# Performance work log

Measured on AMD Instinct MI355X. Metric: run time of the kernel, lower is better.

## Reference

```python
import jax, jax.numpy as jnp
import numpy as np

NEG = -1e30  # finite stand-in for -inf so softmax grads stay clean


def setup_inputs() -> dict:
    key = jax.random.key(0)
    k1, k2 = jax.random.split(key)
    C, D = 8192, 512
    gt_class_embeddings = jax.random.normal(k1, (C, D), dtype=jnp.float32)
    w = jax.random.normal(k2, (C, D), dtype=jnp.float32)
    return {"gt_class_embeddings": gt_class_embeddings, "w": w}


def reference(gt_class_embeddings, w):
    # L2-normalize class embeddings, cosine-similarity matrix S (diag == 1)
    G = gt_class_embeddings / jnp.linalg.norm(gt_class_embeddings, axis=-1, keepdims=True)
    S = G @ G.T  # [C, C]
    C = S.shape[0]
    off_diag = ~jnp.eye(C, dtype=bool)

    # seSoftmax: per-row softmax over entries != 1 (off-diagonal); diagonal stays 1
    P = jax.nn.softmax(jnp.where(off_diag, S, NEG), axis=-1)
    S2 = jnp.where(off_diag, P, 1.0)

    # argsort(-S2)[1] == most similar (diag value 1 always ranks first),
    # argsort(-S2)[-1] == least similar == row min (softmax values < 1)
    ms = jnp.argmax(jnp.where(off_diag, S2, NEG), axis=-1)  # [C]
    ls = jnp.argmin(jnp.where(off_diag, S2, -NEG), axis=-1)  # [C]

    rows = jnp.arange(C)
    margin = S2[rows, ms] - S2[rows, ls]  # [C]

    d_ms = jnp.sqrt(jnp.sum((w - w[ms]) ** 2, axis=-1))  # [C]
    d_ls = jnp.sqrt(jnp.sum((w - w[ls]) ** 2, axis=-1))  # [C]

    loss = jnp.mean(jnp.maximum(0.0, d_ms - d_ls + margin))
    return loss
```

## Files before the change

kernel.cpp:

```cpp
#include <hip/hip_runtime.h>
#include <math.h>

#define CDIM 8192
#define DDIM 512
#define NEGF -3.0e38f
#define POSF  3.0e38f

#define BM 128
#define NSLOT (CDIM / BM)

typedef __attribute__((ext_vector_type(8))) short bf16x8;
typedef __attribute__((ext_vector_type(4))) float f32x4;

__device__ __forceinline__ unsigned short f2bf(float x) {
    unsigned int u = __float_as_uint(x);
    u += 0x7fffu + ((u >> 16) & 1u);
    return (unsigned short)(u >> 16);
}
__device__ __forceinline__ float bf2f(unsigned short h) {
    return __uint_as_float(((unsigned int)h) << 16);
}
__device__ __forceinline__ void gld16(const void* g, void* l) {
    __builtin_amdgcn_global_load_lds(
        (__attribute__((address_space(1))) void*)(void*)g,
        (__attribute__((address_space(3))) void*)l, 16, 0, 0);
}

__global__ __launch_bounds__(256) void k_prep(const float* __restrict__ g,
                                              unsigned short* __restrict__ hi,
                                              unsigned short* __restrict__ lo) {
    const int wave = threadIdx.x >> 6;
    const int lane = threadIdx.x & 63;
    const int row = blockIdx.x * 4 + wave;
    const float4* src = (const float4*)(g + (size_t)row * DDIM);
    const float4 a = src[lane * 2];
    const float4 b = src[lane * 2 + 1];
    float s = a.x * a.x + a.y * a.y + a.z * a.z + a.w * a.w +
              b.x * b.x + b.y * b.y + b.z * b.z + b.w * b.w;
#pragma unroll
    for (int m = 1; m < 64; m <<= 1) s += __shfl_xor(s, m, 64);
    const float rn = rsqrtf(s);
    const float y[8] = {a.x * rn, a.y * rn, a.z * rn, a.w * rn,
                        b.x * rn, b.y * rn, b.z * rn, b.w * rn};
    unsigned int hv[4], lv[4];
#pragma unroll
    for (int i = 0; i < 4; ++i) {
        const unsigned short h0 = f2bf(y[2 * i]);
        const unsigned short h1 = f2bf(y[2 * i + 1]);
        const unsigned short l0 = f2bf(y[2 * i] - bf2f(h0));
        const unsigned short l1 = f2bf(y[2 * i + 1] - bf2f(h1));
        hv[i] = (unsigned int)h0 | ((unsigned int)h1 << 16);
        lv[i] = (unsigned int)l0 | ((unsigned int)l1 << 16);
    }
    uint4* dh = (uint4*)(hi + (size_t)row * DDIM + lane * 8);
    uint4* dl = (uint4*)(lo + (size_t)row * DDIM + lane * 8);
    *dh = make_uint4(hv[0], hv[1], hv[2], hv[3]);
    *dl = make_uint4(lv[0], lv[1], lv[2], lv[3]);
}

__global__ __launch_bounds__(256, 3) void k_simstats(
    const unsigned short* __restrict__ ghi, const unsigned short* __restrict__ glo,
    float* __restrict__ pmax, float* __restrict__ pmin, float* __restrict__ pZ,
    int* __restrict__ pamax, int* __restrict__ pamin) {
    __shared__ unsigned short SH[4 * BM * 32];
    unsigned short* Ahi = SH;
    unsigned short* Alo = SH + 4096;
    unsigned short* Bhi = SH + 8192;
    unsigned short* Blo = SH + 12288;
    const int t = threadIdx.x;
    const int wave = t >> 6;
    const int lane = t & 63;
    const int lanelo = lane & 15;
    const int quad = lane >> 4;
    const int wr = wave & 1;
    const int wc = wave >> 1;

    const int bid = blockIdx.x;
    const int xcd = bid & 7;
    const int off = bid >> 3;
    int I, J, ntiles;
    if (off < 4) {
        const int d = xcd * 4 + off;
        I = 2 * d; J = I; ntiles = 2;
    } else {
        const int e = xcd * 252 + (off - 4);
        int Jf = (int)((1.0f + sqrtf(1.0f + 8.0f * (float)e)) * 0.5f);
        while ((Jf * (Jf - 1)) / 2 > e) --Jf;
        while (((Jf + 1) * Jf) / 2 <= e) ++Jf;
        J = Jf; I = e - (Jf * (Jf - 1)) / 2;
        ntiles = 1;
    }

    const int srow = t >> 2;
    const int scolb = ((t & 3) ^ ((t >> 3) & 3)) << 4;
    char* lAh = (char*)Ahi + t * 16;
    char* lAl = (char*)Alo + t * 16;
    char* lBh = (char*)Bhi + t * 16;
    char* lBl = (char*)Blo + t * 16;

    const int fsl = (quad ^ ((lanelo >> 1) & 3)) << 3;
    const int aoff = (wr * 64 + lanelo) * 32 + fsl;
    const int boff = (wc * 64 + lanelo) * 32 + fsl;

    float* rm  = (float*)SH;
    float* rz  = rm + 256;
    float* rmn = rz + 256;
    int*   ra  = (int*)(rmn + 256);
    int*   ran = ra + 256;
    float* cm  = (float*)Bhi;
    float* cz  = cm + 256;
    float* cmn = cz + 256;
    int*   ca  = (int*)(cmn + 256);
    int*   can = ca + 256;

    for (int tl = 0; tl < ntiles; ++tl) {
        const int Ie = I + tl, Je = J + tl;
        const int i0 = Ie * BM;
        const int j0 = Je * BM;
        const bool isdiag = (Ie == Je);

        f32x4 acc[4][4];
#pragma unroll
        for (int rt = 0; rt < 4; ++rt)
#pragma unroll
            for (int ct = 0; ct < 4; ++ct)
                acc[rt][ct] = (f32x4){0.f, 0.f, 0.f, 0.f};

        const char* baseAh = (const char*)ghi + (size_t)(i0 + srow) * 1024 + scolb;
        const char* baseAl = (const char*)glo + (size_t)(i0 + srow) * 1024 + scolb;
        const char* baseBh = (const char*)ghi + (size_t)(j0 + srow) * 1024 + scolb;
        const char* baseBl = (const char*)glo + (size_t)(j0 + srow) * 1024 + scolb;

        for (int k0 = 0; k0 < DDIM; k0 += 32) {
            __syncthreads();
#pragma unroll
            for (int q = 0; q < 2; ++q) {
                const size_t roff = (size_t)q * 64 * 1024 + k0 * 2;
                gld16(baseAh + roff, lAh + q * 4096);
                gld16(baseAl + roff, lAl + q * 4096);
                gld16(baseBh + roff, lBh + q * 4096);
                gld16(baseBl + roff, lBl + q * 4096);
            }
            __syncthreads();
            bf16x8 ah[4], al[4];
#pragma unroll
            for (int rt = 0; rt < 4; ++rt) {
                ah[rt] = *(const bf16x8*)&Ahi[aoff + rt * 512];
                al[rt] = *(const bf16x8*)&Alo[aoff + rt * 512];
            }
#pragma unroll
            for (int ct = 0; ct < 4; ++ct) {
                const bf16x8 bh = *(const bf16x8*)&Bhi[boff + ct * 512];
                const bf16x8 bl = *(const bf16x8*)&Blo[boff + ct * 512];
#pragma unroll
                for (int rt = 0; rt < 4; ++rt) {
                    acc[rt][ct] = __builtin_amdgcn_mfma_f32_16x16x32_bf16(
                        ah[rt], bh, acc[rt][ct], 0, 0, 0);
                    acc[rt][ct] = __builtin_amdgcn_mfma_f32_16x16x32_bf16(
                        ah[rt], bl, acc[rt][ct], 0, 0, 0);
                    acc[rt][ct] = __builtin_amdgcn_mfma_f32_16x16x32_bf16(
                        al[rt], bh, acc[rt][ct], 0, 0, 0);
                }
            }
        }

        __syncthreads();

#pragma unroll
        for (int rt = 0; rt < 4; ++rt) {
#pragma unroll
            for (int r = 0; r < 4; ++r) {
                const int lrow = wr * 64 + rt * 16 + quad * 4 + r;
                float tmax = NEGF; int targ = 0;
                float tmin = POSF; int targn = 0;
                if (isdiag) {
                    const int gi = i0 + lrow;
#pragma unroll
                    for (int ct = 0; ct < 4; ++ct) {
                        const int gj = j0 + wc * 64 + ct * 16 + lanelo;
                        const float v = acc[rt][ct][r];
                        const bool dg = (gj == gi);
                        const float vM = dg ? NEGF : v;
                        const float vm = dg ? POSF : v;
                        if (vM > tmax) { tmax = vM; targ = gj; }
                        if (vm < tmin) { tmin = vm; targn = gj; }
                    }
                } else {
#pragma unroll
                    for (int ct = 0; ct < 4; ++ct) {
                        const int gj = j0 + wc * 64 + ct * 16 + lanelo;
                        const float v = acc[rt][ct][r];
                        if (v > tmax) { tmax = v; targ = gj; }
                        if (v < tmin) { tmin = v; targn = gj; }
                    }
                }
#pragma unroll
                for (int msk = 1; msk < 16; msk <<= 1) {
                    const float v2 = __shfl_xor(tmax, msk, 64);
                    const int i2 = __shfl_xor(targ, msk, 64);
                    if (v2 > tmax) { tmax = v2; targ = i2; }
                    const float v3 = __shfl_xor(tmin, msk, 64);
                    const int i3 = __shfl_xor(targn, msk, 64);
                    if (v3 < tmin) { tmin = v3; targn = i3; }
                }
                if (lanelo == 0) {
                    const int o = wc * 128 + lrow;
                    rm[o] = tmax; rmn[o] = tmin;
                    ra[o] = targ; ran[o] = targn;
                }
            }
        }

        if (!isdiag) {
#pragma unroll
            for (int ct = 0; ct < 4; ++ct) {
                const int lcol = wc * 64 + ct * 16 + lanelo;
                float tmax = NEGF; int targ = 0;
                float tmin = POSF; int targn = 0;
#pragma unroll
                for (int rt = 0; rt < 4; ++rt)
#pragma unroll
                    for (int r = 0; r < 4; ++r) {
                        const int gi = i0 + wr * 64 + rt * 16 + quad * 4 + r;
                        const float v = acc[rt][ct][r];
                        if (v > tmax) { tmax = v; targ = gi; }
                        if (v < tmin) { tmin = v; targn = gi; }
                    }
#pragma unroll
                for (int msk = 16; msk < 64; msk <<= 1) {
                    const float m2 = __shfl_xor(tmax, msk, 64);
                    const int i2 = __shfl_xor(targ, msk, 64);
                    if (m2 > tmax) { tmax = m2; targ = i2; }
                    const float mn2 = __shfl_xor(tmin, msk, 64);
                    const int in2 = __shfl_xor(targn, msk, 64);
                    if (mn2 < tmin) { tmin = mn2; targn = in2; }
                }
                if (quad == 0) {
                    const int o = wr * 128 + lcol;
                    cm[o] = tmax; cmn[o] = tmin;
                    ca[o] = targ; can[o] = targn;
                }
            }
        }

#pragma unroll
        for (int rt = 0; rt < 4; ++rt)
#pragma unroll
            for (int ct = 0; ct < 4; ++ct)
#pragma unroll
                for (int r = 0; r < 4; ++r)
                    acc[rt][ct][r] = __expf(acc[rt][ct][r] - 1.f);
        if (isdiag && wr == wc) {
#pragma unroll
            for (int rt = 0; rt < 4; ++rt)
#pragma unroll
                for (int r = 0; r < 4; ++r)
                    if (lanelo == quad * 4 + r) acc[rt][rt][r] = 0.f;
        }

#pragma unroll
        for (int rt = 0; rt < 4; ++rt)
#pragma unroll
            for (int r = 0; r < 4; ++r) {
                float s = acc[rt][0][r] + acc[rt][1][r] +
                          acc[rt][2][r] + acc[rt][3][r];
#pragma unroll
                for (int msk = 1; msk < 16; msk <<= 1) s += __shfl_xor(s, msk, 64);
                if (lanelo == 0)
                    rz[wc * 128 + wr * 64 + rt * 16 + quad * 4 + r] = s;
            }

        if (!isdiag) {
#pragma unroll
            for (int ct = 0; ct < 4; ++ct) {
                float s = 0.f;
#pragma unroll
                for (int rt = 0; rt < 4; ++rt)
                    s += acc[rt][ct][0] + acc[rt][ct][1] +
                         acc[rt][ct][2] + acc[rt][ct][3];
#pragma unroll
                for (int msk = 16; msk < 64; msk <<= 1) s += __shfl_xor(s, msk, 64);
                if (quad == 0)
                    cz[wr * 128 + wc * 64 + ct * 16 + lanelo] = s;
            }
        }

        __syncthreads();

        if (t < BM) {
            const float m0 = rm[t], m1 = rm[128 + t];
            float vmax = m0; int imax = ra[t];
            if (m1 > vmax) { vmax = m1; imax = ra[128 + t]; }
            float vmin = rmn[t]; int imin = ran[t];
            if (rmn[128 + t] < vmin) { vmin = rmn[128 + t]; imin = ran[128 + t]; }
            const size_t o = (size_t)Je * CDIM + i0 + t;
            pmax[o] = vmax; pmin[o] = vmin; pZ[o] = rz[t] + rz[128 + t];
            pamax[o] = imax; pamin[o] = imin;
        } else if (!isdiag) {
            const int tt = t - BM;
            const float m0 = cm[tt], m1 = cm[128 + tt];
            float vmax = m0; int imax = ca[tt];
            if (m1 > vmax) { vmax = m1; imax = ca[128 + tt]; }
            float vmin = cmn[tt]; int imin = can[tt];
            if (cmn[128 + tt] < vmin) { vmin = cmn[128 + tt]; imin = can[128 + tt]; }
            const size_t o = (size_t)Ie * CDIM + j0 + tt;
            pmax[o] = vmax; pmin[o] = vmin; pZ[o] = cz[tt] + cz[128 + tt];
            pamax[o] = imax; pamin[o] = imin;
        }
    }
}

__global__ __launch_bounds__(256) void k_merge(
    const float* __restrict__ pmax, const float* __restrict__ pmin,
    const float* __restrict__ pZ, const int* __restrict__ pamax,
    const int* __restrict__ pamin, float* __restrict__ margin,
    int* __restrict__ ms, int* __restrict__ ls) {
    const int row = blockIdx.x * 256 + threadIdx.x;
    float M = NEGF; int a = 0;
    float mn = POSF; int b = 0;
    float Z = 0.f;
    for (int s = 0; s < NSLOT; ++s) {
        const size_t o = (size_t)s * CDIM + row;
        const float v = pmax[o];
        const int ia = pamax[o];
        const float u = pmin[o];
        const int ib = pamin[o];
        Z += pZ[o];
        if (v > M) { M = v; a = ia; }
        if (u < mn) { mn = u; b = ib; }
    }
    margin[row] = (1.f - __expf(mn - M)) * __expf(M - 1.f) / Z;
    ms[row] = a;
    ls[row] = b;
}

__global__ __launch_bounds__(256) void k_dist(
    const float* __restrict__ w, const float* __restrict__ margin,
    const int* __restrict__ ms, const int* __restrict__ ls,
    float* __restrict__ vals) {
    const int wave = threadIdx.x >> 6;
    const int lane = threadIdx.x & 63;
    const int row = blockIdx.x * 4 + wave;
    const int jm = ms[row], jl = ls[row];
    const float4* wi = (const float4*)(w + (size_t)row * DDIM);
    const float4* wm = (const float4*)(w + (size_t)jm * DDIM);
    const float4* wl = (const float4*)(w + (size_t)jl * DDIM);
    float sm = 0.f, sl = 0.f;
#pragma unroll
    for (int h = 0; h < 2; ++h) {
        const int idx = h * 64 + lane;
        const float4 x = wi[idx];
        const float4 y = wm[idx];
        const float4 c = wl[idx];
        float d;
        d = x.x - y.x; sm = fmaf(d, d, sm);
        d = x.y - y.y; sm = fmaf(d, d, sm);
        d = x.z - y.z; sm = fmaf(d, d, sm);
        d = x.w - y.w; sm = fmaf(d, d, sm);
        d = x.x - c.x; sl = fmaf(d, d, sl);
        d = x.y - c.y; sl = fmaf(d, d, sl);
        d = x.z - c.z; sl = fmaf(d, d, sl);
        d = x.w - c.w; sl = fmaf(d, d, sl);
    }
#pragma unroll
    for (int msk = 1; msk < 64; msk <<= 1) {
        sm += __shfl_xor(sm, msk, 64);
        sl += __shfl_xor(sl, msk, 64);
    }
    if (lane == 0) {
        const float val = sqrtf(sm) - sqrtf(sl) + margin[row];
        vals[row] = val > 0.f ? val : 0.f;
    }
}

__global__ __launch_bounds__(256) void k_final(const float* __restrict__ vals,
                                               float* __restrict__ out) {
    __shared__ float red[256];
    float s = 0.f;
    for (int i = threadIdx.x; i < CDIM; i += 256) s += vals[i];
    red[threadIdx.x] = s;
    __syncthreads();
#pragma unroll
    for (int k = 128; k > 0; k >>= 1) {
        if (threadIdx.x < (unsigned)k) red[threadIdx.x] += red[threadIdx.x + k];
        __syncthreads();
    }
    if (threadIdx.x == 0) out[0] = red[0] * (1.0f / CDIM);
}

extern "C" void kernel_launch(void* const* d_in, const int* in_sizes, int n_in,
                              void* d_out, int out_size, void* d_ws, size_t ws_size,
                              hipStream_t stream) {
    const float* g = (const float*)d_in[0];
    const float* w = (const float*)d_in[1];
    float* out = (float*)d_out;

    unsigned short* ghi = (unsigned short*)d_ws;
    unsigned short* glo = ghi + (size_t)CDIM * DDIM;
    float* p = (float*)(glo + (size_t)CDIM * DDIM);
    float* pmax = p;      p += (size_t)NSLOT * CDIM;
    float* pmin = p;      p += (size_t)NSLOT * CDIM;
    float* pZ = p;        p += (size_t)NSLOT * CDIM;
    int* pamax = (int*)p; p += (size_t)NSLOT * CDIM;
    int* pamin = (int*)p; p += (size_t)NSLOT * CDIM;
    float* vals = p;      p += CDIM;
    float* margin = p;    p += CDIM;
    int* ms = (int*)p;    p += CDIM;
    int* ls = (int*)p;    p += CDIM;

    k_prep<<<CDIM / 4, 256, 0, stream>>>(g, ghi, glo);
    k_simstats<<<2048, 256, 0, stream>>>(ghi, glo, pmax, pmin, pZ, pamax, pamin);
    k_merge<<<CDIM / 256, 256, 0, stream>>>(pmax, pmin, pZ, pamax, pamin,
                                            margin, ms, ls);
    k_dist<<<CDIM / 4, 256, 0, stream>>>(w, margin, ms, ls, vals);
    k_final<<<1, 256, 0, stream>>>(vals, out);
}
```

Baseline: 249.8 us.

## Remap symmetric tile schedule into XCD-local 8x8 super-blocks for L2 reuse

Replaces the triangular linear tile enumeration with a super-block schedule. Each XCD handles 8x8 blocks of 128-row tiles (diagonal super-triangles or off-diagonal super-blocks from a constant table), so tiles sharing operand rows run on the same XCD's L2. Diagonal tiles now get one block each instead of pairs, and the grid grows to 2112 with some blocks exiting early. The aim is fewer L2 misses on the bf16 hi/lo operand loads, at the cost of extra launched blocks and some load imbalance across XCDs.

```diff
diff --git a/kernel.cpp b/kernel.cpp
--- a/kernel.cpp
+++ b/kernel.cpp
@@ -58,10 +58,42 @@
     *dl = make_uint4(lv[0], lv[1], lv[2], lv[3]);
 }
 
+__device__ __constant__ unsigned char OSUP[28] = {
+    1, 2, 10,   3, 11, 19,   4, 12, 20,   28, 5, 13,
+    21, 29, 37, 6,   14, 22, 30, 38,   46, 7, 15, 23,   31, 39, 47, 55};
+
 __global__ __launch_bounds__(256, 3) void k_simstats(
     const unsigned short* __restrict__ ghi, const unsigned short* __restrict__ glo,
     float* __restrict__ pmax, float* __restrict__ pmin, float* __restrict__ pZ,
     int* __restrict__ pamax, int* __restrict__ pamin) {
+    const int bid = blockIdx.x;
+    const int xcd = bid & 7;
+    const int off = bid >> 3;
+    int I, J;
+    if (xcd < 4) {
+        if (off < 72) {
+            const int s = xcd * 2 + (off >= 36);
+            const int u = (off >= 36) ? off - 36 : off;
+            int jj = 0;
+            while ((jj + 1) * (jj + 2) / 2 <= u) ++jj;
+            const int ii = u - jj * (jj + 1) / 2;
+            I = s * 8 + ii; J = s * 8 + jj;
+        } else {
+            const int sup = (off - 72) >> 6;
+            const int u = (off - 72) & 63;
+            const int code = OSUP[xcd * 3 + sup];
+            I = (code >> 3) * 8 + (u & 7);
+            J = (code & 7) * 8 + (u >> 3);
+        }
+    } else {
+        if (off >= 256) return;
+        const int sup = off >> 6;
+        const int u = off & 63;
+        const int code = OSUP[12 + (xcd - 4) * 4 + sup];
+        I = (code >> 3) * 8 + (u & 7);
+        J = (code & 7) * 8 + (u >> 3);
+    }
+
     __shared__ unsigned short SH[4 * BM * 32];
     unsigned short* Ahi = SH;
     unsigned short* Alo = SH + 4096;
@@ -75,22 +107,6 @@
     const int wr = wave & 1;
     const int wc = wave >> 1;
 
-    const int bid = blockIdx.x;
-    const int xcd = bid & 7;
-    const int off = bid >> 3;
-    int I, J, ntiles;
-    if (off < 4) {
-        const int d = xcd * 4 + off;
-        I = 2 * d; J = I; ntiles = 2;
-    } else {
-        const int e = xcd * 252 + (off - 4);
-        int Jf = (int)((1.0f + sqrtf(1.0f + 8.0f * (float)e)) * 0.5f);
-        while ((Jf * (Jf - 1)) / 2 > e) --Jf;
-        while (((Jf + 1) * Jf) / 2 <= e) ++Jf;
-        J = Jf; I = e - (Jf * (Jf - 1)) / 2;
-        ntiles = 1;
-    }
-
     const int srow = t >> 2;
     const int scolb = ((t & 3) ^ ((t >> 3) & 3)) << 4;
     char* lAh = (char*)Ahi + t * 16;
@@ -113,200 +129,197 @@
     int*   ca  = (int*)(cmn + 256);
     int*   can = ca + 256;
 
-    for (int tl = 0; tl < ntiles; ++tl) {
-        const int Ie = I + tl, Je = J + tl;
-        const int i0 = Ie * BM;
-        const int j0 = Je * BM;
-        const bool isdiag = (Ie == Je);
-
-        f32x4 acc[4][4];
+    const int i0 = I * BM;
+    const int j0 = J * BM;
+    const bool isdiag = (I == J);
+
+    f32x4 acc[4][4];
+#pragma unroll
+    for (int rt = 0; rt < 4; ++rt)
+#pragma unroll
+        for (int ct = 0; ct < 4; ++ct)
+            acc[rt][ct] = (f32x4){0.f, 0.f, 0.f, 0.f};
+
+    const char* baseAh = (const char*)ghi + (size_t)(i0 + srow) * 1024 + scolb;
+    const char* baseAl = (const char*)glo + (size_t)(i0 + srow) * 1024 + scolb;
+    const char* baseBh = (const char*)ghi + (size_t)(j0 + srow) * 1024 + scolb;
+    const char* baseBl = (const char*)glo + (size_t)(j0 + srow) * 1024 + scolb;
+
+    for (int k0 = 0; k0 < DDIM; k0 += 32) {
+        __syncthreads();
+#pragma unroll
+        for (int q = 0; q < 2; ++q) {
+            const size_t roff = (size_t)q * 64 * 1024 + k0 * 2;
+            gld16(baseAh + roff, lAh + q * 4096);
+            gld16(baseAl + roff, lAl + q * 4096);
+            gld16(baseBh + roff, lBh + q * 4096);
+            gld16(baseBl + roff, lBl + q * 4096);
+        }
+        __syncthreads();
+        bf16x8 ah[4], al[4];
+#pragma unroll
+        for (int rt = 0; rt < 4; ++rt) {
+            ah[rt] = *(const bf16x8*)&Ahi[aoff + rt * 512];
+            al[rt] = *(const bf16x8*)&Alo[aoff + rt * 512];
+        }
+#pragma unroll
+        for (int ct = 0; ct < 4; ++ct) {
+            const bf16x8 bh = *(const bf16x8*)&Bhi[boff + ct * 512];
+            const bf16x8 bl = *(const bf16x8*)&Blo[boff + ct * 512];
+#pragma unroll
+            for (int rt = 0; rt < 4; ++rt) {
+                acc[rt][ct] = __builtin_amdgcn_mfma_f32_16x16x32_bf16(
+                    ah[rt], bh, acc[rt][ct], 0, 0, 0);
+                acc[rt][ct] = __builtin_amdgcn_mfma_f32_16x16x32_bf16(
+                    ah[rt], bl, acc[rt][ct], 0, 0, 0);
+                acc[rt][ct] = __builtin_amdgcn_mfma_f32_16x16x32_bf16(
+                    al[rt], bh, acc[rt][ct], 0, 0, 0);
+            }
+        }
+    }
+
+    __syncthreads();
+
+#pragma unroll
+    for (int rt = 0; rt < 4; ++rt) {
+#pragma unroll
+        for (int r = 0; r < 4; ++r) {
+            const int lrow = wr * 64 + rt * 16 + quad * 4 + r;
+            float tmax = NEGF; int targ = 0;
+            float tmin = POSF; int targn = 0;
+            if (isdiag) {
+                const int gi = i0 + lrow;
+#pragma unroll
+                for (int ct = 0; ct < 4; ++ct) {
+                    const int gj = j0 + wc * 64 + ct * 16 + lanelo;
+                    const float v = acc[rt][ct][r];
+                    const bool dg = (gj == gi);
+                    const float vM = dg ? NEGF : v;
+                    const float vm = dg ? POSF : v;
+                    if (vM > tmax) { tmax = vM; targ = gj; }
+                    if (vm < tmin) { tmin = vm; targn = gj; }
+                }
+            } else {
+#pragma unroll
+                for (int ct = 0; ct < 4; ++ct) {
+                    const int gj = j0 + wc * 64 + ct * 16 + lanelo;
+                    const float v = acc[rt][ct][r];
+                    if (v > tmax) { tmax = v; targ = gj; }
+                    if (v < tmin) { tmin = v; targn = gj; }
+                }
+            }
+#pragma unroll
+            for (int msk = 1; msk < 16; msk <<= 1) {
+                const float v2 = __shfl_xor(tmax, msk, 64);
+                const int i2 = __shfl_xor(targ, msk, 64);
+                if (v2 > tmax) { tmax = v2; targ = i2; }
+                const float v3 = __shfl_xor(tmin, msk, 64);
+                const int i3 = __shfl_xor(targn, msk, 64);
+                if (v3 < tmin) { tmin = v3; targn = i3; }
+            }
+            if (lanelo == 0) {
+                const int o = wc * 128 + lrow;
+                rm[o] = tmax; rmn[o] = tmin;
+                ra[o] = targ; ran[o] = targn;
+            }
+        }
+    }
+
+    if (!isdiag) {
+#pragma unroll
+        for (int ct = 0; ct < 4; ++ct) {
+            const int lcol = wc * 64 + ct * 16 + lanelo;
+            float tmax = NEGF; int targ = 0;
+            float tmin = POSF; int targn = 0;
+#pragma unroll
+            for (int rt = 0; rt < 4; ++rt)
+#pragma unroll
+                for (int r = 0; r < 4; ++r) {
+                    const int gi = i0 + wr * 64 + rt * 16 + quad * 4 + r;
+                    const float v = acc[rt][ct][r];
+                    if (v > tmax) { tmax = v; targ = gi; }
+                    if (v < tmin) { tmin = v; targn = gi; }
+                }
+#pragma unroll
+            for (int msk = 16; msk < 64; msk <<= 1) {
+                const float m2 = __shfl_xor(tmax, msk, 64);
+                const int i2 = __shfl_xor(targ, msk, 64);
+                if (m2 > tmax) { tmax = m2; targ = i2; }
+                const float mn2 = __shfl_xor(tmin, msk, 64);
+                const int in2 = __shfl_xor(targn, msk, 64);
+                if (mn2 < tmin) { tmin = mn2; targn = in2; }
+            }
+            if (quad == 0) {
+                const int o = wr * 128 + lcol;
+                cm[o] = tmax; cmn[o] = tmin;
+                ca[o] = targ; can[o] = targn;
+            }
+        }
+    }
+
+#pragma unroll
+    for (int rt = 0; rt < 4; ++rt)
+#pragma unroll
+        for (int ct = 0; ct < 4; ++ct)
+#pragma unroll
+            for (int r = 0; r < 4; ++r)
+                acc[rt][ct][r] = __expf(acc[rt][ct][r] - 1.f);
+    if (isdiag && wr == wc) {
 #pragma unroll
         for (int rt = 0; rt < 4; ++rt)
 #pragma unroll
-            for (int ct = 0; ct < 4; ++ct)
-                acc[rt][ct] = (f32x4){0.f, 0.f, 0.f, 0.f};
-
-        const char* baseAh = (const char*)ghi + (size_t)(i0 + srow) * 1024 + scolb;
-        const char* baseAl = (const char*)glo + (size_t)(i0 + srow) * 1024 + scolb;
-        const char* baseBh = (const char*)ghi + (size_t)(j0 + srow) * 1024 + scolb;
-        const char* baseBl = (const char*)glo + (size_t)(j0 + srow) * 1024 + scolb;
-
-        for (int k0 = 0; k0 < DDIM; k0 += 32) {
-            __syncthreads();
-#pragma unroll
-            for (int q = 0; q < 2; ++q) {
-                const size_t roff = (size_t)q * 64 * 1024 + k0 * 2;
-                gld16(baseAh + roff, lAh + q * 4096);
-                gld16(baseAl + roff, lAl + q * 4096);
-                gld16(baseBh + roff, lBh + q * 4096);
-                gld16(baseBl + roff, lBl + q * 4096);
-            }
-            __syncthreads();
-            bf16x8 ah[4], al[4];
-#pragma unroll
-            for (int rt = 0; rt < 4; ++rt) {
-                ah[rt] = *(const bf16x8*)&Ahi[aoff + rt * 512];
-                al[rt] = *(const bf16x8*)&Alo[aoff + rt * 512];
-            }
-#pragma unroll
-            for (int ct = 0; ct < 4; ++ct) {
-                const bf16x8 bh = *(const bf16x8*)&Bhi[boff + ct * 512];
-                const bf16x8 bl = *(const bf16x8*)&Blo[boff + ct * 512];
-#pragma unroll
-                for (int rt = 0; rt < 4; ++rt) {
-                    acc[rt][ct] = __builtin_amdgcn_mfma_f32_16x16x32_bf16(
-                        ah[rt], bh, acc[rt][ct], 0, 0, 0);
-                    acc[rt][ct] = __builtin_amdgcn_mfma_f32_16x16x32_bf16(
-                        ah[rt], bl, acc[rt][ct], 0, 0, 0);
-                    acc[rt][ct] = __builtin_amdgcn_mfma_f32_16x16x32_bf16(
-                        al[rt], bh, acc[rt][ct], 0, 0, 0);
-                }
-            }
-        }
-
-        __syncthreads();
-
-#pragma unroll
-        for (int rt = 0; rt < 4; ++rt) {
-#pragma unroll
-            for (int r = 0; r < 4; ++r) {
-                const int lrow = wr * 64 + rt * 16 + quad * 4 + r;
-                float tmax = NEGF; int targ = 0;
-                float tmin = POSF; int targn = 0;
-                if (isdiag) {
-                    const int gi = i0 + lrow;
-#pragma unroll
-                    for (int ct = 0; ct < 4; ++ct) {
-                        const int gj = j0 + wc * 64 + ct * 16 + lanelo;
-                        const float v = acc[rt][ct][r];
-                        const bool dg = (gj == gi);
-                        const float vM = dg ? NEGF : v;
-                        const float vm = dg ? POSF : v;
-                        if (vM > tmax) { tmax = vM; targ = gj; }
-                        if (vm < tmin) { tmin = vm; targn = gj; }
-                    }
-                } else {
-#pragma unroll
-                    for (int ct = 0; ct < 4; ++ct) {
-                        const int gj = j0 + wc * 64 + ct * 16 + lanelo;
-                        const float v = acc[rt][ct][r];
-                        if (v > tmax) { tmax = v; targ = gj; }
-                        if (v < tmin) { tmin = v; targn = gj; }
-                    }
-                }
-#pragma unroll
-                for (int msk = 1; msk < 16; msk <<= 1) {
-                    const float v2 = __shfl_xor(tmax, msk, 64);
-                    const int i2 = __shfl_xor(targ, msk, 64);
-                    if (v2 > tmax) { tmax = v2; targ = i2; }
-                    const float v3 = __shfl_xor(tmin, msk, 64);
-                    const int i3 = __shfl_xor(targn, msk, 64);
-                    if (v3 < tmin) { tmin = v3; targn = i3; }
-                }
-                if (lanelo == 0) {
-                    const int o = wc * 128 + lrow;
-                    rm[o] = tmax; rmn[o] = tmin;
-                    ra[o] = targ; ran[o] = targn;
-                }
-            }
-        }
-
-        if (!isdiag) {
-#pragma unroll
-            for (int ct = 0; ct < 4; ++ct) {
-                const int lcol = wc * 64 + ct * 16 + lanelo;
-                float tmax = NEGF; int targ = 0;
-                float tmin = POSF; int targn = 0;
-#pragma unroll
-                for (int rt = 0; rt < 4; ++rt)
-#pragma unroll
-                    for (int r = 0; r < 4; ++r) {
-                        const int gi = i0 + wr * 64 + rt * 16 + quad * 4 + r;
-                        const float v = acc[rt][ct][r];
-                        if (v > tmax) { tmax = v; targ = gi; }
-                        if (v < tmin) { tmin = v; targn = gi; }
-                    }
-#pragma unroll
-                for (int msk = 16; msk < 64; msk <<= 1) {
-                    const float m2 = __shfl_xor(tmax, msk, 64);
-                    const int i2 = __shfl_xor(targ, msk, 64);
-                    if (m2 > tmax) { tmax = m2; targ = i2; }
-                    const float mn2 = __shfl_xor(tmin, msk, 64);
-                    const int in2 = __shfl_xor(targn, msk, 64);
-                    if (mn2 < tmin) { tmin = mn2; targn = in2; }
-                }
-                if (quad == 0) {
-                    const int o = wr * 128 + lcol;
-                    cm[o] = tmax; cmn[o] = tmin;
-                    ca[o] = targ; can[o] = targn;
-                }
-            }
-        }
-
-#pragma unroll
-        for (int rt = 0; rt < 4; ++rt)
-#pragma unroll
-            for (int ct = 0; ct < 4; ++ct)
-#pragma unroll
-                for (int r = 0; r < 4; ++r)
-                    acc[rt][ct][r] = __expf(acc[rt][ct][r] - 1.f);
-        if (isdiag && wr == wc) {
+            for (int r = 0; r < 4; ++r)
+                if (lanelo == quad * 4 + r) acc[rt][rt][r] = 0.f;
+    }
+
+#pragma unroll
+    for (int rt = 0; rt < 4; ++rt)
+#pragma unroll
+        for (int r = 0; r < 4; ++r) {
+            float s = acc[rt][0][r] + acc[rt][1][r] +
+                      acc[rt][2][r] + acc[rt][3][r];
+#pragma unroll
+            for (int msk = 1; msk < 16; msk <<= 1) s += __shfl_xor(s, msk, 64);
+            if (lanelo == 0)
+                rz[wc * 128 + wr * 64 + rt * 16 + quad * 4 + r] = s;
+        }
+
+    if (!isdiag) {
+#pragma unroll
+        for (int ct = 0; ct < 4; ++ct) {
+            float s = 0.f;
 #pragma unroll
             for (int rt = 0; rt < 4; ++rt)
-#pragma unroll
-                for (int r = 0; r < 4; ++r)
-                    if (lanelo == quad * 4 + r) acc[rt][rt][r] = 0.f;
-        }
-
-#pragma unroll
-        for (int rt = 0; rt < 4; ++rt)
-#pragma unroll
-            for (int r = 0; r < 4; ++r) {
-                float s = acc[rt][0][r] + acc[rt][1][r] +
-                          acc[rt][2][r] + acc[rt][3][r];
-#pragma unroll
-                for (int msk = 1; msk < 16; msk <<= 1) s += __shfl_xor(s, msk, 64);
-                if (lanelo == 0)
-                    rz[wc * 128 + wr * 64 + rt * 16 + quad * 4 + r] = s;
-            }
-
-        if (!isdiag) {
-#pragma unroll
-            for (int ct = 0; ct < 4; ++ct) {
-                float s = 0.f;
-#pragma unroll
-                for (int rt = 0; rt < 4; ++rt)
-                    s += acc[rt][ct][0] + acc[rt][ct][1] +
-                         acc[rt][ct][2] + acc[rt][ct][3];
-#pragma unroll
-                for (int msk = 16; msk < 64; msk <<= 1) s += __shfl_xor(s, msk, 64);
-                if (quad == 0)
-                    cz[wr * 128 + wc * 64 + ct * 16 + lanelo] = s;
-            }
-        }
-
-        __syncthreads();
-
-        if (t < BM) {
-            const float m0 = rm[t], m1 = rm[128 + t];
-            float vmax = m0; int imax = ra[t];
-            if (m1 > vmax) { vmax = m1; imax = ra[128 + t]; }
-            float vmin = rmn[t]; int imin = ran[t];
-            if (rmn[128 + t] < vmin) { vmin = rmn[128 + t]; imin = ran[128 + t]; }
-            const size_t o = (size_t)Je * CDIM + i0 + t;
-            pmax[o] = vmax; pmin[o] = vmin; pZ[o] = rz[t] + rz[128 + t];
-            pamax[o] = imax; pamin[o] = imin;
-        } else if (!isdiag) {
-            const int tt = t - BM;
-            const float m0 = cm[tt], m1 = cm[128 + tt];
-            float vmax = m0; int imax = ca[tt];
-            if (m1 > vmax) { vmax = m1; imax = ca[128 + tt]; }
-            float vmin = cmn[tt]; int imin = can[tt];
-            if (cmn[128 + tt] < vmin) { vmin = cmn[128 + tt]; imin = can[128 + tt]; }
-            const size_t o = (size_t)Ie * CDIM + j0 + tt;
-            pmax[o] = vmax; pmin[o] = vmin; pZ[o] = cz[tt] + cz[128 + tt];
-            pamax[o] = imax; pamin[o] = imin;
-        }
+                s += acc[rt][ct][0] + acc[rt][ct][1] +
+                     acc[rt][ct][2] + acc[rt][ct][3];
+#pragma unroll
+            for (int msk = 16; msk < 64; msk <<= 1) s += __shfl_xor(s, msk, 64);
+            if (quad == 0)
+                cz[wr * 128 + wc * 64 + ct * 16 + lanelo] = s;
+        }
+    }
+
+    __syncthreads();
+
+    if (t < BM) {
+        const float m0 = rm[t], m1 = rm[128 + t];
+        float vmax = m0; int imax = ra[t];
+        if (m1 > vmax) { vmax = m1; imax = ra[128 + t]; }
+        float vmin = rmn[t]; int imin = ran[t];
+        if (rmn[128 + t] < vmin) { vmin = rmn[128 + t]; imin = ran[128 + t]; }
+        const size_t o = (size_t)J * CDIM + i0 + t;
+        pmax[o] = vmax; pmin[o] = vmin; pZ[o] = rz[t] + rz[128 + t];
+        pamax[o] = imax; pamin[o] = imin;
+    } else if (!isdiag) {
+        const int tt = t - BM;
+        const float m0 = cm[tt], m1 = cm[128 + tt];
+        float vmax = m0; int imax = ca[tt];
+        if (m1 > vmax) { vmax = m1; imax = ca[128 + tt]; }
+        float vmin = cmn[tt]; int imin = can[tt];
+        if (cmn[128 + tt] < vmin) { vmin = cmn[128 + tt]; imin = can[128 + tt]; }
+        const size_t o = (size_t)I * CDIM + j0 + tt;
+        pmax[o] = vmax; pmin[o] = vmin; pZ[o] = cz[tt] + cz[128 + tt];
+        pamax[o] = imax; pamin[o] = imin;
     }
 }
 
@@ -409,7 +422,7 @@
     int* ls = (int*)p;    p += CDIM;
 
     k_prep<<<CDIM / 4, 256, 0, stream>>>(g, ghi, glo);
-    k_simstats<<<2048, 256, 0, stream>>>(ghi, glo, pmax, pmin, pZ, pamax, pamin);
+    k_simstats<<<2112, 256, 0, stream>>>(ghi, glo, pmax, pmin, pZ, pamax, pamin);
     k_merge<<<CDIM / 256, 256, 0, stream>>>(pmax, pmin, pZ, pamax, pamin,
                                             margin, ms, ls);
     k_dist<<<CDIM / 4, 256, 0, stream>>>(w, margin, ms, ls, vals);
```

Result: faster. 244.7 us (-2.1%).
